# Performance work log

Measured on AMD Instinct MI355X. Metric: run time of the kernel, lower is better.

## Reference

```python
import jax, jax.numpy as jnp
import numpy as np

N_ITER = 2
BIG = 1e16  # distance assigned to out-of-range superpixel neighbors (zero affinity)


def reference(x, stoken_size):
    B, C, H, W = x.shape
    sh = sw = int(stoken_size)
    nh, nw = H // sh, W // sw
    ns = nh * nw          # num_spixels
    P = H * W             # n_pixel

    pix = x.reshape(B, C, P)  # (B,C,P)
    # initial centroids: adaptive_avg_pool2d == block mean for divisible sizes
    spix = x.reshape(B, C, nh, sh, nw, sw).mean(axis=(3, 5)).reshape(B, C, ns)

    # init label map (nearest interpolation of the ns-label grid to HxW)
    ly = jnp.arange(H) // sh
    lx = jnp.arange(W) // sw
    init_label = (ly[:, None] * nw + lx[None, :]).reshape(-1)  # (P,)

    # 9-neighbor relative superpixel offsets
    rel = jnp.array([-nw - 1, -nw, -nw + 1, -1, 0, 1, nw - 1, nw, nw + 1])
    sidx = init_label[None, :] + rel[:, None]          # (9,P)
    valid = (sidx >= 0) & (sidx < ns)                  # same mask as get_abs_indices
    sidx_c = jnp.clip(sidx, 0, ns - 1)                 # safe gather index
    cols = jnp.broadcast_to(jnp.arange(P)[None, :], (9, P))
    bidx = jnp.broadcast_to(sidx_c[None], (B, 9, P))

    pn = (pix ** 2).sum(axis=1)   # (B,P)
    abs_aff = jnp.zeros((B, ns, P), x.dtype)
    for k in range(N_ITER):
        # pairwise squared distance pixel <-> 9 candidate superpixels
        sn = (spix ** 2).sum(axis=1)                        # (B,ns)
        dots = jnp.einsum('bcs,bcp->bsp', spix, pix)        # (B,ns,P)
        cross = jnp.take_along_axis(dots, bidx, axis=1)     # (B,9,P)
        sng = sn[:, sidx_c]                                 # (B,9,P)
        dist = pn[:, None, :] - 2.0 * cross + sng           # (B,9,P)
        dist = jnp.where(valid[None], dist, jnp.asarray(BIG, x.dtype))
        aff = jax.nn.softmax(-dist, axis=1) * valid[None]   # (B,9,P)
        # dense sparse-scatter: abs_aff[b, sidx[k,p], p] += aff[b,k,p]
        abs_aff = jnp.zeros((B, ns, P), x.dtype).at[:, sidx_c, cols].add(aff)
        if k < N_ITER - 1:
            num = jnp.einsum('bsp,bcp->bcs', abs_aff, pix)             # (B,C,ns)
            spix = num / (abs_aff.sum(axis=2)[:, None, :] + 1e-16)
    # entire ssn_iter runs under torch.no_grad in the original
    return (jax.lax.stop_gradient(abs_aff), ns)


def setup_inputs() -> dict:
    key = jax.random.key(0)
    x = jax.random.normal(key, (4, 64, 256, 256), dtype=jnp.float32)
    return {"x": x, "stoken_size": 16}
```

## Files before the change

kernel.cpp:

```cpp
#include <hip/hip_runtime.h>

#define BB 4
#define CCH 64
#define HH 256
#define WW 256
#define PP (HH*WW)
#define NS 256
#define NW 16


__global__ __launch_bounds__(256) void kA_spix_init(const float* __restrict__ x,
                                                    float* __restrict__ spix) {
    int blk = blockIdx.x;
    int i = blk & 15;
    int c = (blk >> 4) & 63;
    int b = blk >> 10;
    int t = threadIdx.x;
    const float* base = x + ((size_t)(b*CCH + c))*PP + (size_t)i*16*WW + t;
    float s = 0.f;
    #pragma unroll
    for (int r = 0; r < 16; ++r) s += base[(size_t)r*WW];
    #pragma unroll
    for (int off = 8; off; off >>= 1) s += __shfl_down(s, off, 16);
    if ((t & 15) == 0) {
        int j = t >> 4;
        spix[((size_t)b*NS + (i*16 + j))*CCH + c] = s * (1.f/256.f);
    }
}

__global__ __launch_bounds__(256) void kF_fused(const float* __restrict__ x,
                                                const float* __restrict__ spix,
                                                float* __restrict__ partial,
                                                float* __restrict__ wpart) {
    __shared__ float sp[9][64];
    __shared__ float sn[9];
    __shared__ float affL[9][260];
    __shared__ float pixT[32][257];
    float (*red)[9][33] = (float(*)[9][33])&pixT[0][0];

    int blk = blockIdx.x;
    int l = blk & 255, b = blk >> 8;
    int by = l >> 4, bx = l & 15;
    int t = threadIdx.x;

    for (int idx = t; idx < 9*64; idx += 256) {
        int k = idx >> 6, c = idx & 63;
        int rel = (k/3 - 1)*16 + (k % 3) - 1;
        int s = l + rel;
        float v = 0.f;
        if (s >= 0 && s < NS) v = spix[((size_t)b*NS + s)*CCH + c];
        sp[k][c] = v;
    }
    __syncthreads();
    if (t < 9) {
        float s = 0.f;
        #pragma unroll 8
        for (int c = 0; c < CCH; ++c) { float v = sp[t][c]; s += v*v; }
        sn[t] = s;
    }
    __syncthreads();

    int ty = t >> 4, tx = t & 15;
    int gp = (by*16 + ty)*WW + bx*16 + tx;
    const float* px = x + (size_t)b*CCH*PP + gp;

    float cross[9];
    #pragma unroll
    for (int k = 0; k < 9; ++k) cross[k] = 0.f;
    float pn = 0.f;
    for (int c = 0; c < CCH; ++c) {
        float v = px[(size_t)c*PP];
        pn += v*v;
        #pragma unroll
        for (int k = 0; k < 9; ++k) cross[k] += sp[k][c] * v;
    }

    float e[9];
    float m = -1e30f;
    #pragma unroll
    for (int k = 0; k < 9; ++k) {
        int rel = (k/3 - 1)*16 + (k % 3) - 1;
        int s = l + rel;
        bool valid = (s >= 0) && (s < NS);
        float z = -(pn - 2.f*cross[k] + sn[k]);
        e[k] = valid ? z : -3.0e38f;
        if (valid && z > m) m = z;
    }
    float sum = 0.f;
    #pragma unroll
    for (int k = 0; k < 9; ++k) {
        float v = (e[k] > -2.9e38f) ? expf(e[k] - m) : 0.f;
        e[k] = v;
        sum += v;
    }
    float inv = 1.f / sum;
    #pragma unroll
    for (int k = 0; k < 9; ++k) affL[k][t] = e[k] * inv;
    __syncthreads();

    int cl = t & 31, q = t >> 5;
    for (int half = 0; half < 2; ++half) {
        #pragma unroll 4
        for (int ci = 0; ci < 32; ++ci)
            pixT[ci][t] = x[((size_t)(b*CCH + half*32 + ci))*PP + gp];
        __syncthreads();
        float acc[9];
        #pragma unroll
        for (int k = 0; k < 9; ++k) acc[k] = 0.f;
        for (int i = 0; i < 32; ++i) {
            int lp = q*32 + i;
            float v = pixT[cl][lp];
            #pragma unroll
            for (int k = 0; k < 9; ++k) acc[k] += affL[k][lp] * v;
        }
        __syncthreads();
        #pragma unroll
        for (int k = 0; k < 9; ++k) red[q][k][cl] = acc[k];
        __syncthreads();
        for (int tt = t; tt < 9*32; tt += 256) {
            int k = tt >> 5, c2 = tt & 31;
            float s = 0.f;
            #pragma unroll
            for (int qq = 0; qq < 8; ++qq) s += red[qq][k][c2];
            partial[(((size_t)b*9 + k)*NS + l)*CCH + half*32 + c2] = s;
        }
        __syncthreads();
    }
    if (t < 72) {
        int k = t >> 3, seg = t & 7;
        float s = 0.f;
        #pragma unroll
        for (int i = 0; i < 32; ++i) s += affL[k][seg*32 + i];
        red[seg][k][32] = s;
    }
    __syncthreads();
    if (t < 9) {
        float s = 0.f;
        #pragma unroll
        for (int qq = 0; qq < 8; ++qq) s += red[qq][t][32];
        wpart[((size_t)b*9 + t)*NS + l] = s;
    }
}

__global__ __launch_bounds__(256) void kB_aff(const float* __restrict__ x,
                                              const float* __restrict__ spix,
                                              float* __restrict__ aff9) {
    __shared__ float spw[50][65];
    __shared__ float snw[50];
    int blk = blockIdx.x;
    int y = blk & 255;
    int b = blk >> 8;
    int t = threadIdx.x;
    int ly = y >> 4;
    int base = ly*16 - 17;

    for (int idx = t; idx < 50*CCH; idx += 256) {
        int j = idx >> 6, c = idx & 63;
        int g = base + j;
        float v = 0.f;
        if (g >= 0 && g < NS) v = spix[((size_t)b*NS + g)*CCH + c];
        spw[j][c] = v;
    }
    __syncthreads();
    if (t < 50) {
        float s = 0.f;
        #pragma unroll 8
        for (int c = 0; c < CCH; ++c) { float v = spw[t][c]; s += v*v; }
        snw[t] = s;
    }
    __syncthreads();

    int p = y*WW + t;
    const float* px = x + (size_t)b*CCH*PP + p;
    int wl = 17 + (t >> 4);
    int nk[9];
    #pragma unroll
    for (int k = 0; k < 9; ++k) nk[k] = wl + (k/3 - 1)*16 + (k%3 - 1);

    float cross[9];
    #pragma unroll
    for (int k = 0; k < 9; ++k) cross[k] = 0.f;
    float pn = 0.f;
    for (int c = 0; c < CCH; ++c) {
        float v = px[(size_t)c*PP];
        pn += v*v;
        #pragma unroll
        for (int k = 0; k < 9; ++k) cross[k] += spw[nk[k]][c] * v;
    }

    int label = ly*16 + (t >> 4);
    float e[9];
    float m = -1e30f;
    #pragma unroll
    for (int k = 0; k < 9; ++k) {
        int rel = (k/3 - 1)*16 + (k%3 - 1);
        int sidx = label + rel;
        bool valid = (sidx >= 0) && (sidx < NS);
        float z = -(pn - 2.f*cross[k] + snw[nk[k]]);
        e[k] = valid ? z : -3.0e38f;
        if (valid && z > m) m = z;
    }
    float sum = 0.f;
    #pragma unroll
    for (int k = 0; k < 9; ++k) {
        float v = (e[k] > -2.9e38f) ? expf(e[k] - m) : 0.f;
        e[k] = v;
        sum += v;
    }
    float inv = 1.f / sum;
    #pragma unroll
    for (int k = 0; k < 9; ++k)
        aff9[((size_t)b*9 + k)*PP + p] = e[k] * inv;
}

__global__ __launch_bounds__(256) void kD_update(const float* __restrict__ partial,
                                                 const float* __restrict__ wpart,
                                                 float* __restrict__ spix) {
    int gid = blockIdx.x*256 + threadIdx.x;
    int c = gid & 63, s = (gid >> 6) & 255, b = gid >> 14;
    float num = 0.f, den = 0.f;
    #pragma unroll
    for (int k = 0; k < 9; ++k) {
        int rel = (k/3 - 1)*16 + (k%3 - 1);
        int l = s - rel;
        if (l >= 0 && l < NS) {
            num += partial[(((size_t)b*9 + k)*NS + l)*CCH + c];
            den += wpart[((size_t)b*9 + k)*NS + l];
        }
    }
    spix[((size_t)b*NS + s)*CCH + c] = num / (den + 1e-16f);
}

__global__ __launch_bounds__(256) void kE_out(const float* __restrict__ aff9,
                                              float* __restrict__ out,
                                              int out_size) {
    int gid = blockIdx.x*256 + threadIdx.x;
    int row = gid >> 14;
    int col4 = gid & 16383;
    int s = row & 255, b = row >> 8;
    int p = col4 << 2;
    int l = ((p >> 12) << 4) | ((p & 255) >> 4);
    int diff = s - l + 17;
    float4 v = make_float4(0.f, 0.f, 0.f, 0.f);
    if ((unsigned)diff <= 34u && (diff & 15) < 3) {
        int k = (diff >> 4)*3 + (diff & 15);
        const float4* src = (const float4*)(aff9 + ((size_t)b*9 + k)*PP);
        v = src[col4];
    }
    ((float4*)out)[gid] = v;
    if (gid == 0) out[out_size - 1] = 256.0f;
}

extern "C" void kernel_launch(void* const* d_in, const int* in_sizes, int n_in,
                              void* d_out, int out_size, void* d_ws, size_t ws_size,
                              hipStream_t stream) {
    (void)in_sizes; (void)n_in; (void)ws_size;
    const float* x = (const float*)d_in[0];
    float* out = (float*)d_out;
    float* ws = (float*)d_ws;

    float* spix    = ws;
    float* aff9    = spix + (size_t)BB*NS*CCH;
    float* partial = aff9 + (size_t)BB*9*PP;
    float* wpart   = partial + (size_t)BB*9*NS*CCH;

    kA_spix_init<<<BB*CCH*16, 256, 0, stream>>>(x, spix);
    kF_fused<<<BB*NS, 256, 0, stream>>>(x, spix, partial, wpart);
    kD_update<<<BB*NS*CCH/256, 256, 0, stream>>>(partial, wpart, spix);
    kB_aff<<<BB*HH, 256, 0, stream>>>(x, spix, aff9);
    kE_out<<<(BB*NS*PP/4)/256, 256, 0, stream>>>(aff9, out, out_size);
}
```

Before: 127.6 us.

## Fuse affinity and dense output write; keep pixels in registers in fused update

Merges the affinity kernel with the dense output expansion, so each row block stages its 9 affinities in shared memory and writes all 256 superpixel rows directly. This drops the aff9 workspace round trip and one launch. In the fused update kernel, pixel channels are cached in 64 registers instead of being reloaded from global memory, and the reductions now use wavefront shuffles with a smaller shared buffer. The trade-off is higher register pressure from xr[64], which may reduce occupancy.

```diff
diff --git a/kernel.cpp b/kernel.cpp
--- a/kernel.cpp
+++ b/kernel.cpp
@@ -6,7 +6,6 @@
 #define WW 256
 #define PP (HH*WW)
 #define NS 256
-#define NW 16
 
 
 __global__ __launch_bounds__(256) void kA_spix_init(const float* __restrict__ x,
@@ -36,12 +35,14 @@
     __shared__ float sn[9];
     __shared__ float affL[9][260];
     __shared__ float pixT[32][257];
-    float (*red)[9][33] = (float(*)[9][33])&pixT[0][0];
+    __shared__ float red[4][9][33];
+    __shared__ float wsum[4][9];
 
     int blk = blockIdx.x;
     int l = blk & 255, b = blk >> 8;
     int by = l >> 4, bx = l & 15;
     int t = threadIdx.x;
+    int lane = t & 63, w = t >> 6;
 
     for (int idx = t; idx < 9*64; idx += 256) {
         int k = idx >> 6, c = idx & 63;
@@ -64,12 +65,15 @@
     int gp = (by*16 + ty)*WW + bx*16 + tx;
     const float* px = x + (size_t)b*CCH*PP + gp;
 
+    float xr[64];
     float cross[9];
     #pragma unroll
     for (int k = 0; k < 9; ++k) cross[k] = 0.f;
     float pn = 0.f;
+    #pragma unroll
     for (int c = 0; c < CCH; ++c) {
         float v = px[(size_t)c*PP];
+        xr[c] = v;
         pn += v*v;
         #pragma unroll
         for (int k = 0; k < 9; ++k) cross[k] += sp[k][c] * v;
@@ -95,14 +99,27 @@
     }
     float inv = 1.f / sum;
     #pragma unroll
-    for (int k = 0; k < 9; ++k) affL[k][t] = e[k] * inv;
-    __syncthreads();
+    for (int k = 0; k < 9; ++k) { e[k] *= inv; affL[k][t] = e[k]; }
+
+    #pragma unroll
+    for (int k = 0; k < 9; ++k) {
+        float v = e[k];
+        #pragma unroll
+        for (int off = 32; off; off >>= 1) v += __shfl_xor(v, off);
+        if (lane == 0) wsum[w][k] = v;
+    }
+    __syncthreads();
+    if (t < 9) {
+        wpart[((size_t)b*9 + t)*NS + l] =
+            wsum[0][t] + wsum[1][t] + wsum[2][t] + wsum[3][t];
+    }
 
     int cl = t & 31, q = t >> 5;
+    #pragma unroll
     for (int half = 0; half < 2; ++half) {
-        #pragma unroll 4
-        for (int ci = 0; ci < 32; ++ci)
-            pixT[ci][t] = x[((size_t)(b*CCH + half*32 + ci))*PP + gp];
+        if (half) __syncthreads();
+        #pragma unroll
+        for (int ci = 0; ci < 32; ++ci) pixT[ci][t] = xr[half*32 + ci];
         __syncthreads();
         float acc[9];
         #pragma unroll
@@ -113,40 +130,46 @@
             #pragma unroll
             for (int k = 0; k < 9; ++k) acc[k] += affL[k][lp] * v;
         }
-        __syncthreads();
-        #pragma unroll
-        for (int k = 0; k < 9; ++k) red[q][k][cl] = acc[k];
+        #pragma unroll
+        for (int k = 0; k < 9; ++k) acc[k] += __shfl_down(acc[k], 32);
+        if (lane < 32) {
+            #pragma unroll
+            for (int k = 0; k < 9; ++k) red[w][k][cl] = acc[k];
+        }
         __syncthreads();
         for (int tt = t; tt < 9*32; tt += 256) {
             int k = tt >> 5, c2 = tt & 31;
-            float s = 0.f;
-            #pragma unroll
-            for (int qq = 0; qq < 8; ++qq) s += red[qq][k][c2];
+            float s = red[0][k][c2] + red[1][k][c2] + red[2][k][c2] + red[3][k][c2];
             partial[(((size_t)b*9 + k)*NS + l)*CCH + half*32 + c2] = s;
         }
-        __syncthreads();
-    }
-    if (t < 72) {
-        int k = t >> 3, seg = t & 7;
-        float s = 0.f;
-        #pragma unroll
-        for (int i = 0; i < 32; ++i) s += affL[k][seg*32 + i];
-        red[seg][k][32] = s;
-    }
-    __syncthreads();
-    if (t < 9) {
-        float s = 0.f;
-        #pragma unroll
-        for (int qq = 0; qq < 8; ++qq) s += red[qq][t][32];
-        wpart[((size_t)b*9 + t)*NS + l] = s;
-    }
-}
-
-__global__ __launch_bounds__(256) void kB_aff(const float* __restrict__ x,
-                                              const float* __restrict__ spix,
-                                              float* __restrict__ aff9) {
+    }
+}
+
+__global__ __launch_bounds__(256) void kD_update(const float* __restrict__ partial,
+                                                 const float* __restrict__ wpart,
+                                                 float* __restrict__ spix) {
+    int gid = blockIdx.x*256 + threadIdx.x;
+    int c = gid & 63, s = (gid >> 6) & 255, b = gid >> 14;
+    float num = 0.f, den = 0.f;
+    #pragma unroll
+    for (int k = 0; k < 9; ++k) {
+        int rel = (k/3 - 1)*16 + (k%3 - 1);
+        int l = s - rel;
+        if (l >= 0 && l < NS) {
+            num += partial[(((size_t)b*9 + k)*NS + l)*CCH + c];
+            den += wpart[((size_t)b*9 + k)*NS + l];
+        }
+    }
+    spix[((size_t)b*NS + s)*CCH + c] = num / (den + 1e-16f);
+}
+
+__global__ __launch_bounds__(256) void kBE(const float* __restrict__ x,
+                                           const float* __restrict__ spix,
+                                           float* __restrict__ out,
+                                           int out_size) {
     __shared__ float spw[50][65];
     __shared__ float snw[50];
+    __shared__ float affL[9][260];
     int blk = blockIdx.x;
     int y = blk & 255;
     int b = blk >> 8;
@@ -209,46 +232,25 @@
     }
     float inv = 1.f / sum;
     #pragma unroll
-    for (int k = 0; k < 9; ++k)
-        aff9[((size_t)b*9 + k)*PP + p] = e[k] * inv;
-}
-
-__global__ __launch_bounds__(256) void kD_update(const float* __restrict__ partial,
-                                                 const float* __restrict__ wpart,
-                                                 float* __restrict__ spix) {
-    int gid = blockIdx.x*256 + threadIdx.x;
-    int c = gid & 63, s = (gid >> 6) & 255, b = gid >> 14;
-    float num = 0.f, den = 0.f;
-    #pragma unroll
-    for (int k = 0; k < 9; ++k) {
-        int rel = (k/3 - 1)*16 + (k%3 - 1);
-        int l = s - rel;
-        if (l >= 0 && l < NS) {
-            num += partial[(((size_t)b*9 + k)*NS + l)*CCH + c];
-            den += wpart[((size_t)b*9 + k)*NS + l];
-        }
-    }
-    spix[((size_t)b*NS + s)*CCH + c] = num / (den + 1e-16f);
-}
-
-__global__ __launch_bounds__(256) void kE_out(const float* __restrict__ aff9,
-                                              float* __restrict__ out,
-                                              int out_size) {
-    int gid = blockIdx.x*256 + threadIdx.x;
-    int row = gid >> 14;
-    int col4 = gid & 16383;
-    int s = row & 255, b = row >> 8;
-    int p = col4 << 2;
-    int l = ((p >> 12) << 4) | ((p & 255) >> 4);
-    int diff = s - l + 17;
-    float4 v = make_float4(0.f, 0.f, 0.f, 0.f);
-    if ((unsigned)diff <= 34u && (diff & 15) < 3) {
-        int k = (diff >> 4)*3 + (diff & 15);
-        const float4* src = (const float4*)(aff9 + ((size_t)b*9 + k)*PP);
-        v = src[col4];
-    }
-    ((float4*)out)[gid] = v;
-    if (gid == 0) out[out_size - 1] = 256.0f;
+    for (int k = 0; k < 9; ++k) affL[k][t] = e[k] * inv;
+    __syncthreads();
+
+    int w = t >> 6, lane = t & 63;
+    int px4 = lane * 4;
+    int labelbase = ly*16 + (px4 >> 4);
+    float* orow = out + (size_t)b*NS*PP + (size_t)y*WW + px4;
+    #pragma unroll 8
+    for (int r = 0; r < 64; ++r) {
+        int s = w + 4*r;
+        int diff = s - labelbase + 17;
+        float4 v = make_float4(0.f, 0.f, 0.f, 0.f);
+        if ((unsigned)diff <= 34u && (diff & 15) < 3) {
+            int k = (diff >> 4)*3 + (diff & 15);
+            v = *(const float4*)&affL[k][px4];
+        }
+        *(float4*)(orow + (size_t)s*PP) = v;
+    }
+    if (blk == 0 && t == 0) out[out_size - 1] = 256.0f;
 }
 
 extern "C" void kernel_launch(void* const* d_in, const int* in_sizes, int n_in,
@@ -260,13 +262,11 @@
     float* ws = (float*)d_ws;
 
     float* spix    = ws;
-    float* aff9    = spix + (size_t)BB*NS*CCH;
-    float* partial = aff9 + (size_t)BB*9*PP;
+    float* partial = spix + (size_t)BB*NS*CCH;
     float* wpart   = partial + (size_t)BB*9*NS*CCH;
 
     kA_spix_init<<<BB*CCH*16, 256, 0, stream>>>(x, spix);
     kF_fused<<<BB*NS, 256, 0, stream>>>(x, spix, partial, wpart);
     kD_update<<<BB*NS*CCH/256, 256, 0, stream>>>(partial, wpart, spix);
-    kB_aff<<<BB*HH, 256, 0, stream>>>(x, spix, aff9);
-    kE_out<<<(BB*NS*PP/4)/256, 256, 0, stream>>>(aff9, out, out_size);
-}
+    kBE<<<BB*HH, 256, 0, stream>>>(x, spix, out, out_size);
+}
```

New measurement: 114.5 us. -10.2%, faster.
